# Kernel optimization log

Measured on AMD Instinct MI355X. Metric: run time of the kernel, lower is better.

Reference implementation:

```python
import jax, jax.numpy as jnp
import numpy as np

NUM_HEADS = 4
NUM_GROUPS = 32
EPS = 1e-6


def group_norm(x, gamma, beta):
    # x: [b, c, h, w]
    b, c, h, w = x.shape
    xg = x.reshape(b, NUM_GROUPS, c // NUM_GROUPS, h, w)
    mu = xg.mean(axis=(2, 3, 4), keepdims=True)
    var = xg.var(axis=(2, 3, 4), keepdims=True)
    xn = ((xg - mu) * jax.lax.rsqrt(var + EPS)).reshape(b, c, h, w)
    return xn * gamma[None, :, None, None] + beta[None, :, None, None]


def conv1x1(x, W, b):
    # 1x1 conv == per-pixel channel matmul. W: [out_c, in_c], b: [out_c]
    return jnp.einsum('bchw,oc->bohw', x, W) + b[None, :, None, None]


def setup_inputs() -> dict:
    key = jax.random.key(0)
    ks = jax.random.split(key, 8)
    c = 256
    b, h, w = 1, 64, 64
    s = 1.0 / np.sqrt(c)
    return {
        'x_kv': jax.random.normal(ks[0], (b, c, h, w), dtype=jnp.float32),
        'gn_gamma': jnp.ones((c,), dtype=jnp.float32),
        'gn_beta': jnp.zeros((c,), dtype=jnp.float32),
        'Wq': jax.random.normal(ks[1], (c, c), dtype=jnp.float32) * s,
        'bq': jnp.zeros((c,), dtype=jnp.float32),
        'Wk': jax.random.normal(ks[2], (c, c), dtype=jnp.float32) * s,
        'bk': jnp.zeros((c,), dtype=jnp.float32),
        'Wv': jax.random.normal(ks[3], (c, c), dtype=jnp.float32) * s,
        'bv': jnp.zeros((c,), dtype=jnp.float32),
        'Wp': jax.random.normal(ks[4], (c, c), dtype=jnp.float32) * s,
        'bp': jnp.zeros((c,), dtype=jnp.float32),
    }


def reference(x_kv, gn_gamma, gn_beta, Wq, bq, Wk, bk, Wv, bv, Wp, bp):
    b, c, h, w = x_kv.shape
    hd = c // NUM_HEADS
    n = h * w

    h_norm = group_norm(x_kv, gn_gamma, gn_beta)  # self-attn: same norm for q,k,v

    q = conv1x1(h_norm, Wq, bq).reshape(b, NUM_HEADS, hd, n).transpose(0, 1, 3, 2)  # [b,H,n,hd]
    k = conv1x1(h_norm, Wk, bk).reshape(b, NUM_HEADS, hd, n)                        # [b,H,hd,n]
    v = conv1x1(h_norm, Wv, bv).reshape(b, NUM_HEADS, hd, n).transpose(0, 1, 3, 2)  # [b,H,n,hd]

    scores = jnp.einsum('bhnd,bhdm->bhnm', q, k) * (hd ** -0.5)  # [b,H,n,n]
    attn = jax.nn.softmax(scores, axis=-1)
    out = jnp.einsum('bhnm,bhmd->bhnd', attn, v)  # [b,H,n,hd]

    # Faithful to torch: permute(0,2,1,3).contiguous().view(b,c,h,w)
    out = out.transpose(0, 2, 1, 3).reshape(b, c, h, w)
    return x_kv + conv1x1(out, Wp, bp)
```

## Files before the change

kernel.cpp:

```cpp
#include <hip/hip_runtime.h>
#include <hip/hip_bf16.h>

#define NPIX 4096
#define CCH  256
#define HD   64
#define GSIZE 32768

#define QSCALE 0.18033688f

typedef __bf16 bf16x8 __attribute__((ext_vector_type(8)));
typedef __bf16 bf16x4 __attribute__((ext_vector_type(4)));
typedef __bf16 bf16x2 __attribute__((ext_vector_type(2)));
typedef float  f32x4  __attribute__((ext_vector_type(4)));
typedef unsigned int uint32x4 __attribute__((ext_vector_type(4)));

#define XPITCH 264

#if __has_builtin(__builtin_amdgcn_exp2f)
#define EXP2(x) __builtin_amdgcn_exp2f(x)
#else
#define EXP2(x) __expf((x) * 0.6931471805599453f)
#endif


__device__ __forceinline__ unsigned pack_bf16x2(float lo, float hi)
{
    bf16x2 v;
    v[0] = (__bf16)lo;
    v[1] = (__bf16)hi;
    return __builtin_bit_cast(unsigned, v);
}

__global__ __launch_bounds__(256) void stats_wconv(
    const float* __restrict__ X,
    const float* __restrict__ Wq, const float* __restrict__ Wk,
    const float* __restrict__ Wv, const float* __restrict__ Wp,
    float* __restrict__ psum, float* __restrict__ pssq, __bf16* __restrict__ Wb)
{
    const int bid = blockIdx.x, t = threadIdx.x;
    if (bid < 256) {
        const float* base = X + bid * 4096;
        float sum = 0.f, ssq = 0.f;
        #pragma unroll
        for (int k = 0; k < 4; ++k) {
            float4 v = *(const float4*)(base + t * 4 + k * 1024);
            sum += v.x + v.y + v.z + v.w;
            ssq += v.x * v.x + v.y * v.y + v.z * v.z + v.w * v.w;
        }
        #pragma unroll
        for (int off = 1; off < 64; off <<= 1) {
            sum += __shfl_xor(sum, off);
            ssq += __shfl_xor(ssq, off);
        }
        __shared__ float red[2][4];
        const int wv = t >> 6;
        if ((t & 63) == 0) { red[0][wv] = sum; red[1][wv] = ssq; }
        __syncthreads();
        if (t == 0) {
            psum[bid] = red[0][0] + red[0][1] + red[0][2] + red[0][3];
            pssq[bid] = red[1][0] + red[1][1] + red[1][2] + red[1][3];
        }
    } else {
        const int j0 = (bid - 256) * 4096 + t * 16;
        const int m  = j0 >> 16;
        const float* W = (m == 0) ? Wq : (m == 1) ? Wk : (m == 2) ? Wv : Wp;
        const float sc = (m == 0) ? QSCALE : 1.f;
        const int off = j0 & 65535;
        #pragma unroll
        for (int k = 0; k < 4; ++k) {
            float4 v = *(const float4*)(W + off + k * 4);
            bf16x4 o;
            o[0] = (__bf16)(v.x * sc); o[1] = (__bf16)(v.y * sc);
            o[2] = (__bf16)(v.z * sc); o[3] = (__bf16)(v.w * sc);
            *(bf16x4*)(Wb + m * 65536 + off + k * 4) = o;
        }
    }
}

__global__ __launch_bounds__(256) void gn_qkv(
    const float* __restrict__ X, const float* __restrict__ gamma,
    const float* __restrict__ beta,
    const float* __restrict__ psum, const float* __restrict__ pssq,
    const __bf16* __restrict__ Wb,
    const float* __restrict__ bq, const float* __restrict__ bk,
    const float* __restrict__ bv,
    __bf16* __restrict__ Qb, __bf16* __restrict__ Kb, __bf16* __restrict__ Vb)
{
    __shared__ __bf16 tile[64 * XPITCH];
    __shared__ float al[256], bl[256];

    const int t = threadIdx.x, lane = t & 63, wave = t >> 6;
    const int l16 = lane & 15, quad = lane >> 4;
    const int p0 = blockIdx.x * 64;
    const int z = blockIdx.y >> 1, och = blockIdx.y & 1;

    {
        const int g = t >> 3;
        float s = 0.f, q = 0.f;
        #pragma unroll
        for (int j = 0; j < 8; ++j) { s += psum[g * 8 + j]; q += pssq[g * 8 + j]; }
        const float mu  = s * (1.f / GSIZE);
        const float var = q * (1.f / GSIZE) - mu * mu;
        const float a = gamma[t] * rsqrtf(var + 1e-6f);
        al[t] = a;
        bl[t] = beta[t] - mu * a;
    }
    __syncthreads();

    #pragma unroll 4
    for (int i = 0; i < 16; ++i) {
        const int c4 = wave * 64 + i * 4;
        f32x4 a4 = *(const f32x4*)(al + c4);
        f32x4 b4 = *(const f32x4*)(bl + c4);
        bf16x4 pk;
        pk[0] = (__bf16)(X[(c4 + 0) * NPIX + p0 + lane] * a4[0] + b4[0]);
        pk[1] = (__bf16)(X[(c4 + 1) * NPIX + p0 + lane] * a4[1] + b4[1]);
        pk[2] = (__bf16)(X[(c4 + 2) * NPIX + p0 + lane] * a4[2] + b4[2]);
        pk[3] = (__bf16)(X[(c4 + 3) * NPIX + p0 + lane] * a4[3] + b4[3]);
        *(bf16x4*)(tile + lane * XPITCH + c4) = pk;
    }
    __syncthreads();

    const int pw = wave * 16;
    bf16x8 xf[8];
    #pragma unroll
    for (int kc = 0; kc < 8; ++kc)
        xf[kc] = *(const bf16x8*)(tile + (pw + l16) * XPITCH + kc * 32 + quad * 8);

    const __bf16* Wz = Wb + z * 65536;
    const float* bias = (z == 0) ? bq : (z == 1) ? bk : bv;

    if (z < 2) {
        const float qs = (z == 0) ? QSCALE : 1.f;
        __bf16* dst = (z == 0) ? Qb : Kb;
        #pragma unroll
        for (int grp = 0; grp < 2; ++grp) {
            f32x4 acc[4] = {};
            #pragma unroll
            for (int kc = 0; kc < 8; ++kc) {
                #pragma unroll
                for (int u = 0; u < 4; ++u) {
                    bf16x8 wf = *(const bf16x8*)(Wz + (och * 128 + (grp * 4 + u) * 16 + l16) * CCH + kc * 32 + quad * 8);
                    acc[u] = __builtin_amdgcn_mfma_f32_16x16x32_bf16(wf, xf[kc], acc[u], 0, 0, 0);
                }
            }
            #pragma unroll
            for (int u = 0; u < 4; ++u) {
                const int ot = och * 8 + grp * 4 + u;
                f32x4 bz = *(const f32x4*)(bias + och * 128 + (grp * 4 + u) * 16 + quad * 4);
                bf16x4 o;
                o[0] = (__bf16)(acc[u][0] + bz[0] * qs);
                o[1] = (__bf16)(acc[u][1] + bz[1] * qs);
                o[2] = (__bf16)(acc[u][2] + bz[2] * qs);
                o[3] = (__bf16)(acc[u][3] + bz[3] * qs);
                const int head = ot >> 2, dloc = (ot & 3) * 16 + quad * 4;
                *(bf16x4*)(dst + head * (NPIX * HD) + (p0 + pw + l16) * HD + dloc) = o;
            }
        }
    } else {
        #pragma unroll
        for (int grp = 0; grp < 2; ++grp) {
            f32x4 acc[4] = {};
            #pragma unroll
            for (int kc = 0; kc < 8; ++kc) {
                #pragma unroll
                for (int u = 0; u < 4; ++u) {
                    bf16x8 wf = *(const bf16x8*)(Wz + (och * 128 + (grp * 4 + u) * 16 + l16) * CCH + kc * 32 + quad * 8);
                    acc[u] = __builtin_amdgcn_mfma_f32_16x16x32_bf16(xf[kc], wf, acc[u], 0, 0, 0);
                }
            }
            #pragma unroll
            for (int u = 0; u < 4; ++u) {
                const int oc = och * 128 + (grp * 4 + u) * 16 + l16;
                const float bz = bias[oc];
                bf16x4 o;
                o[0] = (__bf16)(acc[u][0] + bz); o[1] = (__bf16)(acc[u][1] + bz);
                o[2] = (__bf16)(acc[u][2] + bz); o[3] = (__bf16)(acc[u][3] + bz);
                *(bf16x4*)(Vb + oc * NPIX + p0 + pw + quad * 4) = o;
            }
        }
    }
}

__global__ __launch_bounds__(256, 1) void attn_mfma(
    const __bf16* __restrict__ Qb, const __bf16* __restrict__ Kb,
    const __bf16* __restrict__ Vb, __bf16* __restrict__ Sb)
{
    __shared__ __align__(16) float co[4 * 64 * 68];
    __shared__ float cl[4 * 64];

    const int t = threadIdx.x, lane = t & 63, wave = t >> 6;
    const int l16 = lane & 15, quad = lane >> 4;

    const int bid  = blockIdx.x;
    const int head = (bid & 7) >> 1;
    const int qt   = ((bid >> 3) << 1) | (bid & 1);
    const int p0   = qt * 64;

    const __bf16* Qh = Qb + head * (NPIX * HD);
    const __bf16* Kh = Kb + head * (NPIX * HD) + (wave * 32 + l16) * HD + quad * 8;
    const __bf16* Vh = Vb + head * (HD * NPIX) + l16 * NPIX + wave * 32 + quad * 8;

    bf16x8 qf[4][2];
    #pragma unroll
    for (int rt = 0; rt < 4; ++rt) {
        const __bf16* qp = Qh + (p0 + rt * 16 + l16) * HD + quad * 8;
        qf[rt][0] = *(const bf16x8*)(qp);
        qf[rt][1] = *(const bf16x8*)(qp + 32);
    }

    bf16x8 ones;
    #pragma unroll
    for (int j = 0; j < 8; ++j) ones[j] = (__bf16)1.0f;

    f32x4 l_acc[4] = {};
    f32x4 o_acc[4][4] = {};

    auto ldK = [&](int it, bf16x8& k0, bf16x8& k1, bf16x8& k2, bf16x8& k3) {
        const __bf16* kp = Kh + it * (128 * HD);
        k0 = *(const bf16x8*)(kp);
        k1 = *(const bf16x8*)(kp + 32);
        k2 = *(const bf16x8*)(kp + 16 * HD);
        k3 = *(const bf16x8*)(kp + 16 * HD + 32);
    };
    auto ldV = [&](int it, bf16x8& v0, bf16x8& v1, bf16x8& v2, bf16x8& v3) {
        const __bf16* vp = Vh + it * 128;
        v0 = *(const bf16x8*)(vp);
        v1 = *(const bf16x8*)(vp + 16 * NPIX);
        v2 = *(const bf16x8*)(vp + 32 * NPIX);
        v3 = *(const bf16x8*)(vp + 48 * NPIX);
    };

    auto qk = [&](bf16x8 k0, bf16x8 k1, bf16x8 k2, bf16x8 k3,
                  f32x4 (&s0)[4], f32x4 (&s1)[4]) {
        #pragma unroll
        for (int rt = 0; rt < 4; ++rt) {
            s0[rt] = f32x4{0.f, 0.f, 0.f, 0.f};
            s1[rt] = f32x4{0.f, 0.f, 0.f, 0.f};
            s0[rt] = __builtin_amdgcn_mfma_f32_16x16x32_bf16(k0, qf[rt][0], s0[rt], 0, 0, 0);
            s0[rt] = __builtin_amdgcn_mfma_f32_16x16x32_bf16(k1, qf[rt][1], s0[rt], 0, 0, 0);
            s1[rt] = __builtin_amdgcn_mfma_f32_16x16x32_bf16(k2, qf[rt][0], s1[rt], 0, 0, 0);
            s1[rt] = __builtin_amdgcn_mfma_f32_16x16x32_bf16(k3, qf[rt][1], s1[rt], 0, 0, 0);
        }
    };

    auto pvx = [&](const f32x4 (&s0)[4], const f32x4 (&s1)[4],
                   bf16x8 v0, bf16x8 v1, bf16x8 v2, bf16x8 v3) {
        #pragma unroll
        for (int rt = 0; rt < 4; ++rt) {
            unsigned a0 = pack_bf16x2(EXP2(s0[rt][0]), EXP2(s0[rt][1]));
            unsigned a1 = pack_bf16x2(EXP2(s0[rt][2]), EXP2(s0[rt][3]));
            unsigned b0 = pack_bf16x2(EXP2(s1[rt][0]), EXP2(s1[rt][1]));
            unsigned b1 = pack_bf16x2(EXP2(s1[rt][2]), EXP2(s1[rt][3]));
            asm("v_permlane32_swap_b32 %0, %1" : "+v"(a0), "+v"(b0));
            asm("v_permlane32_swap_b32 %0, %1" : "+v"(a1), "+v"(b1));
            asm("v_permlane16_swap_b32 %0, %1" : "+v"(a0), "+v"(b0));
            asm("v_permlane16_swap_b32 %0, %1" : "+v"(a1), "+v"(b1));
            uint32x4 w;
            w[0] = a0; w[1] = a1; w[2] = b0; w[3] = b1;
            const bf16x8 bp = __builtin_bit_cast(bf16x8, w);
            l_acc[rt] = __builtin_amdgcn_mfma_f32_16x16x32_bf16(ones, bp, l_acc[rt], 0, 0, 0);
            o_acc[0][rt] = __builtin_amdgcn_mfma_f32_16x16x32_bf16(v0, bp, o_acc[0][rt], 0, 0, 0);
            o_acc[1][rt] = __builtin_amdgcn_mfma_f32_16x16x32_bf16(v1, bp, o_acc[1][rt], 0, 0, 0);
            o_acc[2][rt] = __builtin_amdgcn_mfma_f32_16x16x32_bf16(v2, bp, o_acc[2][rt], 0, 0, 0);
            o_acc[3][rt] = __builtin_amdgcn_mfma_f32_16x16x32_bf16(v3, bp, o_acc[3][rt], 0, 0, 0);
        }
    };

    bf16x8 kA0, kA1, kA2, kA3, vA0, vA1, vA2, vA3;
    bf16x8 kB0, kB1, kB2, kB3, vB0, vB1, vB2, vB3;
    f32x4 sA0[4], sA1[4], sB0[4], sB1[4];

    ldK(0, kA0, kA1, kA2, kA3);
    ldV(0, vA0, vA1, vA2, vA3);

    #pragma unroll 1
    for (int it = 0; it < 32; it += 2) {
        ldK(it + 1, kB0, kB1, kB2, kB3);
        qk(kA0, kA1, kA2, kA3, sA0, sA1);
        ldV(it + 1, vB0, vB1, vB2, vB3);
        pvx(sA0, sA1, vA0, vA1, vA2, vA3);
        if (it + 2 < 32) ldK(it + 2, kA0, kA1, kA2, kA3);
        qk(kB0, kB1, kB2, kB3, sB0, sB1);
        if (it + 2 < 32) ldV(it + 2, vA0, vA1, vA2, vA3);
        pvx(sB0, sB1, vB0, vB1, vB2, vB3);
    }

    #pragma unroll
    for (int dt = 0; dt < 4; ++dt)
        #pragma unroll
        for (int rt = 0; rt < 4; ++rt)
            *(f32x4*)(co + wave * 4352 + (rt * 16 + l16) * 68 + dt * 16 + quad * 4) = o_acc[dt][rt];
    if (quad == 0) {
        #pragma unroll
        for (int rt = 0; rt < 4; ++rt)
            cl[wave * 64 + rt * 16 + l16] = l_acc[rt][0];
    }
    __syncthreads();

    {
        const int row = t >> 2, dc = (t & 3) * 16;
        const float l = cl[row] + cl[64 + row] + cl[128 + row] + cl[192 + row];
        const float inv = 1.f / l;
        f32x4 s[4];
        #pragma unroll
        for (int j = 0; j < 4; ++j) {
            s[j] = f32x4{0.f, 0.f, 0.f, 0.f};
            #pragma unroll
            for (int w = 0; w < 4; ++w)
                s[j] += *(const f32x4*)(co + w * 4352 + row * 68 + dc + j * 4);
        }
        bf16x8 o1, o2;
        #pragma unroll
        for (int j = 0; j < 4; ++j) {
            o1[j]     = (__bf16)(s[0][j] * inv);
            o1[j + 4] = (__bf16)(s[1][j] * inv);
            o2[j]     = (__bf16)(s[2][j] * inv);
            o2[j + 4] = (__bf16)(s[3][j] * inv);
        }
        __bf16* dst = Sb + (p0 + row) * CCH + head * HD + dc;
        *(bf16x8*)(dst)     = o1;
        *(bf16x8*)(dst + 8) = o2;
    }
}

__global__ __launch_bounds__(256) void gemm_proj(
    const __bf16* __restrict__ Sb, const __bf16* __restrict__ Wpb,
    const float* __restrict__ bias, const float* __restrict__ X,
    float* __restrict__ Out)
{
    __shared__ __bf16 Bs[32 * XPITCH];

    const int t = threadIdx.x, lane = t & 63, wave = t >> 6;
    const int l16 = lane & 15, quad = lane >> 4;
    const int p0  = blockIdx.x * 32;
    const int och = blockIdx.y;

    #pragma unroll
    for (int pg = 0; pg < 4; ++pg) {
        bf16x8 v = *(const bf16x8*)(Sb + t * NPIX + p0 + pg * 8);
        #pragma unroll
        for (int j = 0; j < 8; ++j)
            Bs[(pg * 8 + j) * XPITCH + t] = v[j];
    }
    __syncthreads();

    const int pixset = wave & 1, ocset = wave >> 1;
    bf16x8 af[8];
    #pragma unroll
    for (int kc = 0; kc < 8; ++kc)
        af[kc] = *(const bf16x8*)(Bs + (pixset * 16 + l16) * XPITCH + kc * 32 + quad * 8);

    #pragma unroll
    for (int u = 0; u < 4; ++u) {
        f32x4 acc = {};
        const int oc_t = och * 128 + ocset * 64 + u * 16;
        #pragma unroll
        for (int kc = 0; kc < 8; ++kc) {
            bf16x8 wf = *(const bf16x8*)(Wpb + (oc_t + l16) * CCH + kc * 32 + quad * 8);
            acc = __builtin_amdgcn_mfma_f32_16x16x32_bf16(af[kc], wf, acc, 0, 0, 0);
        }
        const int oc  = oc_t + l16;
        const int pix = p0 + pixset * 16 + quad * 4;
        const float bz = bias[oc];
        f32x4 r4 = *(const f32x4*)(X + oc * NPIX + pix);
        f32x4 y;
        y[0] = acc[0] + bz + r4[0];
        y[1] = acc[1] + bz + r4[1];
        y[2] = acc[2] + bz + r4[2];
        y[3] = acc[3] + bz + r4[3];
        *(f32x4*)(Out + oc * NPIX + pix) = y;
    }
}

extern "C" void kernel_launch(void* const* d_in, const int* in_sizes, int n_in,
                              void* d_out, int out_size, void* d_ws, size_t ws_size,
                              hipStream_t stream)
{
    const float* x     = (const float*)d_in[0];
    const float* gamma = (const float*)d_in[1];
    const float* beta  = (const float*)d_in[2];
    const float* Wq    = (const float*)d_in[3];
    const float* bq    = (const float*)d_in[4];
    const float* Wk    = (const float*)d_in[5];
    const float* bk    = (const float*)d_in[6];
    const float* Wv    = (const float*)d_in[7];
    const float* bv    = (const float*)d_in[8];
    const float* Wp    = (const float*)d_in[9];
    const float* bp    = (const float*)d_in[10];
    float* out = (float*)d_out;

    char* ws = (char*)d_ws;
    float*  psum = (float*)(ws);
    float*  pssq = (float*)(ws + 1024);
    __bf16* Wb   = (__bf16*)(ws + 65536);
    __bf16* Qb   = (__bf16*)(ws + (1 << 20));
    __bf16* Kb   = (__bf16*)(ws + (3 << 20));
    __bf16* Vb   = (__bf16*)(ws + (5 << 20));
    __bf16* Sb   = (__bf16*)(ws + (7 << 20));

    stats_wconv<<<320, 256, 0, stream>>>(x, Wq, Wk, Wv, Wp, psum, pssq, Wb);

    dim3 gq(64, 6);
    gn_qkv<<<gq, 256, 0, stream>>>(x, gamma, beta, psum, pssq, Wb,
                                   bq, bk, bv, Qb, Kb, Vb);

    attn_mfma<<<256, 256, 0, stream>>>(Qb, Kb, Vb, Sb);

    dim3 gp(128, 2);
    gemm_proj<<<gp, 256, 0, stream>>>(Sb, Wb + 3 * 65536, bp, x, out);
}
```

Before: 141.6 us.

## Stage K/V tiles through LDS with async global_load_lds double buffering

The attention kernel now copies each K/V tile into swizzled, double-buffered LDS with direct global-to-LDS loads, where it used to load fragments straight from global memory into registers. Waves read their fragments from LDS after a waitcnt and barrier, and the next tile's copy is issued once compute on the current buffer finishes. This is meant to hide global latency and take pressure off registers. The cost is two block barriers per iteration and a larger LDS footprint, which is reused for the epilogue reduction.

New measurement: 135.8 us. 1.04x faster.

```diff
diff --git a/kernel.cpp b/kernel.cpp
--- a/kernel.cpp
+++ b/kernel.cpp
@@ -29,6 +29,13 @@
     v[0] = (__bf16)lo;
     v[1] = (__bf16)hi;
     return __builtin_bit_cast(unsigned, v);
+}
+
+__device__ __forceinline__ void gload_lds16(const void* g, void* l)
+{
+    __builtin_amdgcn_global_load_lds(
+        (const __attribute__((address_space(1))) void*)g,
+        (__attribute__((address_space(3))) void*)l, 16, 0, 0);
 }
 
 __global__ __launch_bounds__(256) void stats_wconv(
@@ -182,12 +189,17 @@
     }
 }
 
+#define OFFK0 0
+#define OFFK1 16384
+#define OFFV0 32768
+#define OFFV1 49152
+#define SMEMSZ 70656
+
 __global__ __launch_bounds__(256, 1) void attn_mfma(
     const __bf16* __restrict__ Qb, const __bf16* __restrict__ Kb,
     const __bf16* __restrict__ Vb, __bf16* __restrict__ Sb)
 {
-    __shared__ __align__(16) float co[4 * 64 * 68];
-    __shared__ float cl[4 * 64];
+    __shared__ __align__(16) char smem[SMEMSZ];
 
     const int t = threadIdx.x, lane = t & 63, wave = t >> 6;
     const int l16 = lane & 15, quad = lane >> 4;
@@ -198,8 +210,6 @@
     const int p0   = qt * 64;
 
     const __bf16* Qh = Qb + head * (NPIX * HD);
-    const __bf16* Kh = Kb + head * (NPIX * HD) + (wave * 32 + l16) * HD + quad * 8;
-    const __bf16* Vh = Vb + head * (HD * NPIX) + l16 * NPIX + wave * 32 + quad * 8;
 
     bf16x8 qf[4][2];
     #pragma unroll
@@ -216,19 +226,28 @@
     f32x4 l_acc[4] = {};
     f32x4 o_acc[4][4] = {};
 
-    auto ldK = [&](int it, bf16x8& k0, bf16x8& k1, bf16x8& k2, bf16x8& k3) {
-        const __bf16* kp = Kh + it * (128 * HD);
-        k0 = *(const bf16x8*)(kp);
-        k1 = *(const bf16x8*)(kp + 32);
-        k2 = *(const bf16x8*)(kp + 16 * HD);
-        k3 = *(const bf16x8*)(kp + 16 * HD + 32);
+    const int lr3 = lane >> 3, lc3 = lane & 7;
+    const int lr4 = lane >> 4, lc4 = lane & 15;
+    const int kcol = ((lc3 ^ lr3) << 4);
+    const char* Kg = (const char*)(Kb + (head * NPIX) * HD);
+    const char* Vg = (const char*)(Vb + (head * HD) * NPIX);
+
+    auto stageK = [&](int it, int b) {
+        char* dst = smem + (b ? OFFK1 : OFFK0) + wave * 4096;
+        const char* src = Kg + (it * 128 + wave * 32) * 128;
+        #pragma unroll
+        for (int i = 0; i < 4; ++i)
+            gload_lds16(src + (i * 8 + lr3) * 128 + kcol, dst + i * 1024);
     };
-    auto ldV = [&](int it, bf16x8& v0, bf16x8& v1, bf16x8& v2, bf16x8& v3) {
-        const __bf16* vp = Vh + it * 128;
-        v0 = *(const bf16x8*)(vp);
-        v1 = *(const bf16x8*)(vp + 16 * NPIX);
-        v2 = *(const bf16x8*)(vp + 32 * NPIX);
-        v3 = *(const bf16x8*)(vp + 48 * NPIX);
+    auto stageV = [&](int it, int b) {
+        char* dst = smem + (b ? OFFV1 : OFFV0) + wave * 4096;
+        const char* src = Vg + (wave * 16) * (NPIX * 2) + it * 256;
+        #pragma unroll
+        for (int i = 0; i < 4; ++i) {
+            const int d  = i * 4 + lr4;
+            const int sw = (((wave * 16 + d) & 7) << 4);
+            gload_lds16(src + d * (NPIX * 2) + ((lc4 << 4) ^ sw), dst + i * 1024);
+        }
     };
 
     auto qk = [&](bf16x8 k0, bf16x8 k1, bf16x8 k2, bf16x8 k3,
@@ -267,24 +286,44 @@
         }
     };
 
-    bf16x8 kA0, kA1, kA2, kA3, vA0, vA1, vA2, vA3;
-    bf16x8 kB0, kB1, kB2, kB3, vB0, vB1, vB2, vB3;
-    f32x4 sA0[4], sA1[4], sB0[4], sB1[4];
-
-    ldK(0, kA0, kA1, kA2, kA3);
-    ldV(0, vA0, vA1, vA2, vA3);
+    stageK(0, 0); stageV(0, 0);
+    stageK(1, 1); stageV(1, 1);
+
+    const int ksw = ((l16 & 7) << 4);
 
     #pragma unroll 1
-    for (int it = 0; it < 32; it += 2) {
-        ldK(it + 1, kB0, kB1, kB2, kB3);
-        qk(kA0, kA1, kA2, kA3, sA0, sA1);
-        ldV(it + 1, vB0, vB1, vB2, vB3);
-        pvx(sA0, sA1, vA0, vA1, vA2, vA3);
-        if (it + 2 < 32) ldK(it + 2, kA0, kA1, kA2, kA3);
-        qk(kB0, kB1, kB2, kB3, sB0, sB1);
-        if (it + 2 < 32) ldV(it + 2, vA0, vA1, vA2, vA3);
-        pvx(sB0, sB1, vB0, vB1, vB2, vB3);
-    }
+    for (int it = 0; it < 32; ++it) {
+        const int b = it & 1;
+        if (it == 31) asm volatile("s_waitcnt vmcnt(0)" ::: "memory");
+        else          asm volatile("s_waitcnt vmcnt(8)" ::: "memory");
+        __builtin_amdgcn_s_barrier();
+        __builtin_amdgcn_sched_barrier(0);
+
+        const char* bk = smem + (b ? OFFK1 : OFFK0);
+        const char* bv = smem + (b ? OFFV1 : OFFV0);
+
+        const int kr0 = (wave * 32 + l16) * 128;
+        bf16x8 k0 = *(const bf16x8*)(bk + kr0 + ((quad * 16) ^ ksw));
+        bf16x8 k1 = *(const bf16x8*)(bk + kr0 + ((64 + quad * 16) ^ ksw));
+        bf16x8 k2 = *(const bf16x8*)(bk + kr0 + 2048 + ((quad * 16) ^ ksw));
+        bf16x8 k3 = *(const bf16x8*)(bk + kr0 + 2048 + ((64 + quad * 16) ^ ksw));
+        const int vcol = (wave * 64 + quad * 16) ^ ksw;
+        bf16x8 v0 = *(const bf16x8*)(bv + (l16) * 256 + vcol);
+        bf16x8 v1 = *(const bf16x8*)(bv + (16 + l16) * 256 + vcol);
+        bf16x8 v2 = *(const bf16x8*)(bv + (32 + l16) * 256 + vcol);
+        bf16x8 v3 = *(const bf16x8*)(bv + (48 + l16) * 256 + vcol);
+
+        f32x4 s0[4], s1[4];
+        qk(k0, k1, k2, k3, s0, s1);
+        pvx(s0, s1, v0, v1, v2, v3);
+
+        __builtin_amdgcn_sched_barrier(0);
+        __builtin_amdgcn_s_barrier();
+        if (it < 30) { stageK(it + 2, b); stageV(it + 2, b); }
+    }
+
+    float* co = (float*)smem;
+    float* cl = (float*)(smem + 69632);
 
     #pragma unroll
     for (int dt = 0; dt < 4; ++dt)
```
